# Kernel optimization log

Hardware: AMD Instinct MI355X
Metric: run time of the kernel (lower is better)

Reference implementation:

```python
import jax, jax.numpy as jnp
import numpy as np

B, T, D = 8, 2048, 1024  # batch, block_size (== seq len), n_embd


def setup_inputs() -> dict:
    key = jax.random.key(0)
    k1, k2 = jax.random.split(key)
    x = jax.random.normal(k1, (B, T, D), dtype=jnp.float32)
    W_qkv = jax.random.normal(k2, (3 * D, D), dtype=jnp.float32) * 0.02
    b_qkv = jnp.zeros((3 * D,), dtype=jnp.float32)
    ln_w = jnp.ones((D,), dtype=jnp.float32)
    ln_b = jnp.zeros((D,), dtype=jnp.float32)
    return {"x": x, "W_qkv": W_qkv, "b_qkv": b_qkv, "ln_w": ln_w, "ln_b": ln_b}


def reference(x, W_qkv, b_qkv, ln_w, ln_b):
    # qkv projection: Linear(n_embd, 3*n_embd)
    qkv = jnp.einsum('btd,ed->bte', x, W_qkv) + b_qkv  # [B,T,3D]
    q, k, v = jnp.split(qkv, 3, axis=-1)
    # causal linear attention (no softmax)
    scale = np.sqrt(D * T).astype(np.float32)
    scores = jnp.einsum('bid,bjd->bij', q, k) / scale  # [B,T,T]
    mask = jnp.tril(jnp.ones((T, T), dtype=scores.dtype))
    scores = scores * mask
    y = jnp.einsum('bij,bjd->bid', scores, v)  # [B,T,D]
    # LayerNorm over last dim, eps=1e-5
    mu = jnp.mean(y, axis=-1, keepdims=True)
    var = jnp.mean(jnp.square(y - mu), axis=-1, keepdims=True)
    y_hat = (y - mu) * jax.lax.rsqrt(var + 1e-5)
    return y_hat * ln_w + ln_b
```

## Files before the change

kernel.cpp:

```cpp
#include <hip/hip_runtime.h>
#include <hip/hip_bf16.h>
#include <stdint.h>

typedef __attribute__((ext_vector_type(8))) short bf16x8;
typedef __attribute__((ext_vector_type(4))) float f32x4;
typedef __attribute__((ext_vector_type(4))) unsigned short us4;

#define TILE_M 128
#define TILE_N 128
#define TILE_K 32

__device__ __forceinline__ unsigned short f2b(float f) {
  union { float f; unsigned u; } u;
  u.f = f;
  unsigned r = u.u + 0x7fffu + ((u.u >> 16) & 1u);
  return (unsigned short)(r >> 16);
}

__device__ __forceinline__ void gload_lds16(const void* g, void* lds) {
  __builtin_amdgcn_global_load_lds(
      (const __attribute__((address_space(1))) unsigned int*)(uintptr_t)g,
      (__attribute__((address_space(3))) unsigned int*)(uintptr_t)lds,
      16, 0, 0);
}

__device__ __forceinline__ void stage_tile(const unsigned short* __restrict__ g,
                                           long ld, long row0,
                                           unsigned short* lds, int tid) {
  int w = tid >> 6, lane = tid & 63;
#pragma unroll
  for (int j = 0; j < 2; ++j) {
    int o = ((w * 2 + j) << 10) + lane * 16;
    int row = o >> 6;
    int col = (o & 63) >> 1;
    const unsigned short* gp = g + (row0 + row) * ld + col;
    gload_lds16(gp, (char*)lds + ((w * 2 + j) << 10));
  }
}

__global__ __launch_bounds__(256, 2) void gemm1_qkv(
    const unsigned short* __restrict__ A,
    const unsigned short* __restrict__ Bm,
    const float* __restrict__ bias,
    unsigned short* __restrict__ C) {
  __shared__ unsigned short lsA[TILE_M * TILE_K];
  __shared__ unsigned short lsB[TILE_N * TILE_K];
  int tid = threadIdx.x;
  int lane = tid & 63, w = tid >> 6;
  int wr = w >> 1, wc = w & 1;
  long bm0 = (long)blockIdx.y * TILE_M;
  long bn0 = (long)blockIdx.x * TILE_N;
  f32x4 acc[4][4] = {};
  int r = lane & 15, g = lane >> 4;
  for (int kt = 0; kt < 1024 / TILE_K; ++kt) {
    long k0 = (long)kt * TILE_K;
    stage_tile(A + k0, 1024, bm0, lsA, tid);
    stage_tile(Bm + k0, 1024, bn0, lsB, tid);
    __syncthreads();
    bf16x8 aF[4], bF[4];
#pragma unroll
    for (int m = 0; m < 4; ++m)
      aF[m] = *(const bf16x8*)(lsA + (wr * 64 + m * 16 + r) * 32 + g * 8);
#pragma unroll
    for (int n = 0; n < 4; ++n)
      bF[n] = *(const bf16x8*)(lsB + (wc * 64 + n * 16 + r) * 32 + g * 8);
#pragma unroll
    for (int m = 0; m < 4; ++m)
#pragma unroll
      for (int n = 0; n < 4; ++n)
        acc[m][n] = __builtin_amdgcn_mfma_f32_16x16x32_bf16(aF[m], bF[n], acc[m][n], 0, 0, 0);
    __syncthreads();
  }
#pragma unroll
  for (int n = 0; n < 4; ++n) {
    long col = bn0 + wc * 64 + n * 16 + r;
    float bv = bias[col];
#pragma unroll
    for (int m = 0; m < 4; ++m)
#pragma unroll
      for (int j = 0; j < 4; ++j) {
        long row = bm0 + wr * 64 + m * 16 + g * 4 + j;
        C[row * 3072 + col] = f2b(acc[m][n][j] + bv);
      }
  }
}

__global__ __launch_bounds__(256, 2) void gemm2_scores(
    const unsigned short* __restrict__ qkv,
    unsigned short* __restrict__ scores,
    float inv_scale) {
  int bj = blockIdx.x, bi = blockIdx.y, b = blockIdx.z;
  if (bj > bi) return;
  __shared__ unsigned short lsA[TILE_M * TILE_K];
  __shared__ unsigned short lsB[TILE_N * TILE_K];
  int tid = threadIdx.x;
  int lane = tid & 63, w = tid >> 6;
  int wr = w >> 1, wc = w & 1;
  long bm0 = (long)bi * TILE_M;
  long bn0 = (long)bj * TILE_N;
  const unsigned short* A = qkv + (long)b * 2048 * 3072;
  const unsigned short* Bm = qkv + (long)b * 2048 * 3072 + 1024;
  f32x4 acc[4][4] = {};
  int r = lane & 15, g = lane >> 4;
  for (int kt = 0; kt < 1024 / TILE_K; ++kt) {
    long k0 = (long)kt * TILE_K;
    stage_tile(A + k0, 3072, bm0, lsA, tid);
    stage_tile(Bm + k0, 3072, bn0, lsB, tid);
    __syncthreads();
    bf16x8 aF[4], bF[4];
#pragma unroll
    for (int m = 0; m < 4; ++m)
      aF[m] = *(const bf16x8*)(lsA + (wr * 64 + m * 16 + r) * 32 + g * 8);
#pragma unroll
    for (int n = 0; n < 4; ++n)
      bF[n] = *(const bf16x8*)(lsB + (wc * 64 + n * 16 + r) * 32 + g * 8);
#pragma unroll
    for (int m = 0; m < 4; ++m)
#pragma unroll
      for (int n = 0; n < 4; ++n)
        acc[m][n] = __builtin_amdgcn_mfma_f32_16x16x32_bf16(aF[m], bF[n], acc[m][n], 0, 0, 0);
    __syncthreads();
  }
  unsigned short* S = scores + (long)b * 2048 * 2048;
#pragma unroll
  for (int n = 0; n < 4; ++n) {
    long col = bn0 + wc * 64 + n * 16 + r;
#pragma unroll
    for (int m = 0; m < 4; ++m)
#pragma unroll
      for (int j = 0; j < 4; ++j) {
        long row = bm0 + wr * 64 + m * 16 + g * 4 + j;
        float v = acc[m][n][j] * inv_scale;
        if (col > row) v = 0.0f;
        S[row * 2048 + col] = f2b(v);
      }
  }
}

__global__ __launch_bounds__(256, 2) void gemm3_y(
    const unsigned short* __restrict__ scores,
    const unsigned short* __restrict__ vT,
    float* __restrict__ out) {
  int bn = blockIdx.x, bi = blockIdx.y, b = blockIdx.z;
  __shared__ unsigned short lsA[TILE_M * TILE_K];
  __shared__ unsigned short lsB[TILE_N * TILE_K];
  int tid = threadIdx.x;
  int lane = tid & 63, w = tid >> 6;
  int wr = w >> 1, wc = w & 1;
  long bm0 = (long)bi * TILE_M;
  long bn0 = (long)bn * TILE_N;
  const unsigned short* A = scores + (long)b * 2048 * 2048;
  const unsigned short* Bm = vT + (long)b * 1024 * 2048;
  f32x4 acc[4][4] = {};
  int r = lane & 15, g = lane >> 4;
  int KT = (bi + 1) * (TILE_M / TILE_K);
  for (int kt = 0; kt < KT; ++kt) {
    long k0 = (long)kt * TILE_K;
    stage_tile(A + k0, 2048, bm0, lsA, tid);
    stage_tile(Bm + k0, 2048, bn0, lsB, tid);
    __syncthreads();
    bf16x8 aF[4], bF[4];
#pragma unroll
    for (int m = 0; m < 4; ++m)
      aF[m] = *(const bf16x8*)(lsA + (wr * 64 + m * 16 + r) * 32 + g * 8);
#pragma unroll
    for (int n = 0; n < 4; ++n)
      bF[n] = *(const bf16x8*)(lsB + (wc * 64 + n * 16 + r) * 32 + g * 8);
#pragma unroll
    for (int m = 0; m < 4; ++m)
#pragma unroll
      for (int n = 0; n < 4; ++n)
        acc[m][n] = __builtin_amdgcn_mfma_f32_16x16x32_bf16(aF[m], bF[n], acc[m][n], 0, 0, 0);
    __syncthreads();
  }
#pragma unroll
  for (int n = 0; n < 4; ++n) {
    long col = bn0 + wc * 64 + n * 16 + r;
#pragma unroll
    for (int m = 0; m < 4; ++m)
#pragma unroll
      for (int j = 0; j < 4; ++j) {
        long row = bm0 + wr * 64 + m * 16 + g * 4 + j;
        out[((long)b * 2048 + row) * 1024 + col] = acc[m][n][j];
      }
  }
}

__global__ void cvt_f32_bf16(const float* __restrict__ in,
                             unsigned short* __restrict__ out, long n) {
  long i = ((long)blockIdx.x * blockDim.x + threadIdx.x) * 8;
  if (i + 8 > n) return;
  float4 a = *(const float4*)(in + i);
  float4 b = *(const float4*)(in + i + 4);
  bf16x8 o;
  o[0] = (short)f2b(a.x); o[1] = (short)f2b(a.y);
  o[2] = (short)f2b(a.z); o[3] = (short)f2b(a.w);
  o[4] = (short)f2b(b.x); o[5] = (short)f2b(b.y);
  o[6] = (short)f2b(b.z); o[7] = (short)f2b(b.w);
  *(bf16x8*)(out + i) = o;
}

__global__ void transpose_v(const unsigned short* __restrict__ qkv,
                            unsigned short* __restrict__ vT) {
  __shared__ unsigned short tile[64][72];
  int t0 = blockIdx.x * 64, d0 = blockIdx.y * 64, b = blockIdx.z;
  int tid = threadIdx.x;
  int sub = tid & 15, grp = tid >> 4;
#pragma unroll
  for (int it = 0; it < 4; ++it) {
    int tt = it * 16 + grp;
    int dd = sub * 4;
    const unsigned short* src =
        qkv + ((long)(b * 2048 + t0 + tt)) * 3072 + 2048 + d0 + dd;
    *(us4*)&tile[tt][dd] = *(const us4*)src;
  }
  __syncthreads();
#pragma unroll
  for (int it = 0; it < 4; ++it) {
    int dd = it * 16 + grp;
    int ts = sub * 4;
    us4 o;
    o[0] = tile[ts + 0][dd];
    o[1] = tile[ts + 1][dd];
    o[2] = tile[ts + 2][dd];
    o[3] = tile[ts + 3][dd];
    *(us4*)(vT + ((long)b * 1024 + d0 + dd) * 2048 + t0 + ts) = o;
  }
}

__global__ void ln_kernel(float* __restrict__ y, const float* __restrict__ wv,
                          const float* __restrict__ bv) {
  __shared__ float sm[4];
  long row = blockIdx.x;
  int tid = threadIdx.x;
  float4 v = *(const float4*)(y + row * 1024 + tid * 4);
  float s = v.x + v.y + v.z + v.w;
#pragma unroll
  for (int o = 32; o > 0; o >>= 1) s += __shfl_xor(s, o, 64);
  if ((tid & 63) == 0) sm[tid >> 6] = s;
  __syncthreads();
  float mu = (sm[0] + sm[1] + sm[2] + sm[3]) * (1.0f / 1024.0f);
  float dx = v.x - mu, dy = v.y - mu, dz = v.z - mu, dw = v.w - mu;
  float sq = dx * dx + dy * dy + dz * dz + dw * dw;
#pragma unroll
  for (int o = 32; o > 0; o >>= 1) sq += __shfl_xor(sq, o, 64);
  __syncthreads();
  if ((tid & 63) == 0) sm[tid >> 6] = sq;
  __syncthreads();
  float var = (sm[0] + sm[1] + sm[2] + sm[3]) * (1.0f / 1024.0f);
  float inv = rsqrtf(var + 1e-5f);
  float4 w4 = *(const float4*)(wv + tid * 4);
  float4 b4 = *(const float4*)(bv + tid * 4);
  float4 o4;
  o4.x = dx * inv * w4.x + b4.x;
  o4.y = dy * inv * w4.y + b4.y;
  o4.z = dz * inv * w4.z + b4.z;
  o4.w = dw * inv * w4.w + b4.w;
  *(float4*)(y + row * 1024 + tid * 4) = o4;
}

extern "C" void kernel_launch(void* const* d_in, const int* in_sizes, int n_in,
                              void* d_out, int out_size, void* d_ws, size_t ws_size,
                              hipStream_t stream) {
  const float* x   = (const float*)d_in[0];
  const float* W   = (const float*)d_in[1];
  const float* bq  = (const float*)d_in[2];
  const float* lnw = (const float*)d_in[3];
  const float* lnb = (const float*)d_in[4];
  float* out = (float*)d_out;

  char* ws = (char*)d_ws;
  unsigned short* qkv = (unsigned short*)(ws);
  unsigned short* vT  = (unsigned short*)(ws + 100663296L);
  unsigned short* sc  = (unsigned short*)(ws + 134217728L);
  unsigned short* xb  = (unsigned short*)(ws + 134217728L);
  unsigned short* Wb  = (unsigned short*)(ws + 167772160L);

  const float inv_scale = 1.0f / sqrtf(1024.0f * 2048.0f);

  cvt_f32_bf16<<<8192, 256, 0, stream>>>(x, xb, 16384L * 1024);
  cvt_f32_bf16<<<1536, 256, 0, stream>>>(W, Wb, 3072L * 1024);
  gemm1_qkv<<<dim3(24, 128), 256, 0, stream>>>(xb, Wb, bq, qkv);
  transpose_v<<<dim3(32, 16, 8), 256, 0, stream>>>(qkv, vT);
  gemm2_scores<<<dim3(16, 16, 8), 256, 0, stream>>>(qkv, sc, inv_scale);
  gemm3_y<<<dim3(8, 16, 8), 256, 0, stream>>>(sc, vT, out);
  ln_kernel<<<16384, 256, 0, stream>>>(out, lnw, lnb);
}
```

Before: 444.2 us.

## Rewrite GEMMs with 256x256 tiles, swizzled double-buffered LDS and interleaved MFMA pipeline

All three GEMMs now share one core that uses 256x256 output tiles with 512 threads, K=64 stages, XOR-swizzled LDS to avoid bank conflicts, and a double-buffered 128 KB LDS ring. Global-to-LDS loads are issued in quarters between MFMA groups, with explicit waitcnt, barriers and raised scheduling priority so memory overlaps compute. gemm1 also remaps block ids for better L2 locality. The larger tiles cut grid sizes and raise register pressure. The causal gemm3 now has coarser load imbalance, since K is rounded up to 256-row steps.

```diff
diff --git a/kernel.cpp b/kernel.cpp
--- a/kernel.cpp
+++ b/kernel.cpp
@@ -6,9 +6,7 @@
 typedef __attribute__((ext_vector_type(4))) float f32x4;
 typedef __attribute__((ext_vector_type(4))) unsigned short us4;
 
-#define TILE_M 128
-#define TILE_N 128
-#define TILE_K 32
+#define SWZ(L) ((L) ^ ((((L) >> 7) & 7) << 4))
 
 __device__ __forceinline__ unsigned short f2b(float f) {
   union { float f; unsigned u; } u;
@@ -24,112 +22,175 @@
       16, 0, 0);
 }
 
-__device__ __forceinline__ void stage_tile(const unsigned short* __restrict__ g,
-                                           long ld, long row0,
-                                           unsigned short* lds, int tid) {
+__device__ __forceinline__ void stage_half(
+    const unsigned short* __restrict__ Ag, const unsigned short* __restrict__ Bg,
+    long bm0, long bn0, long ldA, long ldB, char* lds, int h, int tid) {
+  int T = h >> 2, q = h & 3;
+  const unsigned short* mat = (q < 2) ? Ag : Bg;
+  long row0 = (q < 2) ? bm0 : bn0;
+  long ld = (q < 2) ? ldA : ldB;
+  char* tile = lds + (long)(T & 1) * 65536 + (q >> 1) * 32768;
   int w = tid >> 6, lane = tid & 63;
 #pragma unroll
   for (int j = 0; j < 2; ++j) {
-    int o = ((w * 2 + j) << 10) + lane * 16;
-    int row = o >> 6;
-    int col = (o & 63) >> 1;
-    const unsigned short* gp = g + (row0 + row) * ld + col;
-    gload_lds16(gp, (char*)lds + ((w * 2 + j) << 10));
-  }
-}
-
-__global__ __launch_bounds__(256, 2) void gemm1_qkv(
-    const unsigned short* __restrict__ A,
-    const unsigned short* __restrict__ Bm,
-    const float* __restrict__ bias,
-    unsigned short* __restrict__ C) {
-  __shared__ unsigned short lsA[TILE_M * TILE_K];
-  __shared__ unsigned short lsB[TILE_N * TILE_K];
+    int P = (q & 1) * 16384 + j * 8192 + w * 1024 + lane * 16;
+    int L = SWZ(P);
+    const unsigned short* gp =
+        mat + (row0 + (L >> 7)) * ld + (long)T * 64 + ((L & 127) >> 1);
+    gload_lds16(gp, tile + (q & 1) * 16384 + j * 8192 + w * 1024);
+  }
+}
+
+__device__ __forceinline__ void readA(const char* tA, int wr, int r, int g,
+                                      bf16x8 (&aF)[8][2]) {
+#pragma unroll
+  for (int m = 0; m < 8; ++m)
+#pragma unroll
+    for (int s = 0; s < 2; ++s) {
+      int L = (wr * 128 + m * 16 + r) * 128 + s * 64 + g * 16;
+      aF[m][s] = *(const bf16x8*)(tA + SWZ(L));
+    }
+}
+
+__device__ __forceinline__ void readB(const char* tB, int wc, int qn, int r, int g,
+                                      bf16x8 (&bF)[2][2]) {
+#pragma unroll
+  for (int n = 0; n < 2; ++n)
+#pragma unroll
+    for (int s = 0; s < 2; ++s) {
+      int L = (wc * 64 + (qn * 2 + n) * 16 + r) * 128 + s * 64 + g * 16;
+      bF[n][s] = *(const bf16x8*)(tB + SWZ(L));
+    }
+}
+
+template <int QM, int QN>
+__device__ __forceinline__ void mfma_quad(f32x4 (&acc)[8][4], bf16x8 (&aF)[8][2],
+                                          bf16x8 (&bF)[2][2]) {
+#pragma unroll
+  for (int s = 0; s < 2; ++s)
+#pragma unroll
+    for (int mm = 0; mm < 4; ++mm)
+#pragma unroll
+      for (int nn = 0; nn < 2; ++nn)
+        acc[QM * 4 + mm][QN * 2 + nn] = __builtin_amdgcn_mfma_f32_16x16x32_bf16(
+            aF[QM * 4 + mm][s], bF[nn][s], acc[QM * 4 + mm][QN * 2 + nn], 0, 0, 0);
+}
+
+#define SBAR() do { __builtin_amdgcn_s_barrier(); __builtin_amdgcn_sched_barrier(0); } while (0)
+
+__device__ __forceinline__ void gemm_core(
+    const unsigned short* __restrict__ Ag, const unsigned short* __restrict__ Bg,
+    long bm0, long bn0, long ldA, long ldB, int KT, char* lds,
+    f32x4 (&acc)[8][4]) {
   int tid = threadIdx.x;
-  int lane = tid & 63, w = tid >> 6;
-  int wr = w >> 1, wc = w & 1;
-  long bm0 = (long)blockIdx.y * TILE_M;
-  long bn0 = (long)blockIdx.x * TILE_N;
-  f32x4 acc[4][4] = {};
+  int w = tid >> 6, lane = tid & 63;
+  int wr = w >> 2, wc = w & 3;
   int r = lane & 15, g = lane >> 4;
-  for (int kt = 0; kt < 1024 / TILE_K; ++kt) {
-    long k0 = (long)kt * TILE_K;
-    stage_tile(A + k0, 1024, bm0, lsA, tid);
-    stage_tile(Bm + k0, 1024, bn0, lsB, tid);
-    __syncthreads();
-    bf16x8 aF[4], bF[4];
-#pragma unroll
-    for (int m = 0; m < 4; ++m)
-      aF[m] = *(const bf16x8*)(lsA + (wr * 64 + m * 16 + r) * 32 + g * 8);
-#pragma unroll
-    for (int n = 0; n < 4; ++n)
-      bF[n] = *(const bf16x8*)(lsB + (wc * 64 + n * 16 + r) * 32 + g * 8);
-#pragma unroll
-    for (int m = 0; m < 4; ++m)
-#pragma unroll
-      for (int n = 0; n < 4; ++n)
-        acc[m][n] = __builtin_amdgcn_mfma_f32_16x16x32_bf16(aF[m], bF[n], acc[m][n], 0, 0, 0);
-    __syncthreads();
-  }
+  int totalH = KT * 4;
+#pragma unroll
+  for (int h = 0; h < 7; ++h)
+    stage_half(Ag, Bg, bm0, bn0, ldA, ldB, lds, h, tid);
+  asm volatile("s_waitcnt vmcnt(6)" ::: "memory");
+  SBAR();
+
+  bf16x8 aF[8][2], bF[2][2];
+  int niter = KT >> 1;
+  for (int it = 0; it < niter; ++it) {
+    bool last = (it == niter - 1);
+    int hb = it * 8 + 7;
+#pragma unroll
+    for (int c = 0; c < 2; ++c) {
+      char* tA = lds + c * 65536;
+      char* tB = tA + 32768;
+      readA(tA, wr, r, g, aF);
+      readB(tB, wc, 0, r, g, bF);
+      if (hb + c * 4 + 0 < totalH)
+        stage_half(Ag, Bg, bm0, bn0, ldA, ldB, lds, hb + c * 4 + 0, tid);
+      SBAR();
+      __builtin_amdgcn_s_setprio(1);
+      mfma_quad<0, 0>(acc, aF, bF);
+      __builtin_amdgcn_s_setprio(0);
+      asm volatile("s_waitcnt lgkmcnt(0)" ::: "memory");
+      __builtin_amdgcn_sched_barrier(0);
+      SBAR();
+      if (hb + c * 4 + 1 < totalH)
+        stage_half(Ag, Bg, bm0, bn0, ldA, ldB, lds, hb + c * 4 + 1, tid);
+      SBAR();
+      __builtin_amdgcn_s_setprio(1);
+      mfma_quad<1, 0>(acc, aF, bF);
+      __builtin_amdgcn_s_setprio(0);
+      SBAR();
+      readB(tB, wc, 1, r, g, bF);
+      if (hb + c * 4 + 2 < totalH)
+        stage_half(Ag, Bg, bm0, bn0, ldA, ldB, lds, hb + c * 4 + 2, tid);
+      SBAR();
+      __builtin_amdgcn_s_setprio(1);
+      mfma_quad<1, 1>(acc, aF, bF);
+      __builtin_amdgcn_s_setprio(0);
+      SBAR();
+      if (hb + c * 4 + 3 < totalH)
+        stage_half(Ag, Bg, bm0, bn0, ldA, ldB, lds, hb + c * 4 + 3, tid);
+      SBAR();
+      __builtin_amdgcn_s_setprio(1);
+      mfma_quad<0, 1>(acc, aF, bF);
+      __builtin_amdgcn_s_setprio(0);
+      if (!last)
+        asm volatile("s_waitcnt vmcnt(6)" ::: "memory");
+      else if (c == 0)
+        asm volatile("s_waitcnt vmcnt(0)" ::: "memory");
+      SBAR();
+    }
+  }
+}
+
+__global__ __launch_bounds__(512, 2) void gemm1_qkv(
+    const unsigned short* __restrict__ A, const unsigned short* __restrict__ Bm,
+    const float* __restrict__ bias, unsigned short* __restrict__ C) {
+  extern __shared__ char smem[];
+  int bid = blockIdx.x;
+  int s = (bid & 7) * 96 + (bid >> 3);
+  long bm0 = (long)(s / 12) * 256;
+  long bn0 = (long)(s % 12) * 256;
+  f32x4 acc[8][4] = {};
+  gemm_core(A, Bm, bm0, bn0, 1024, 1024, 16, smem, acc);
+  int tid = threadIdx.x, w = tid >> 6, lane = tid & 63;
+  int wr = w >> 2, wc = w & 3, r = lane & 15, g = lane >> 4;
 #pragma unroll
   for (int n = 0; n < 4; ++n) {
     long col = bn0 + wc * 64 + n * 16 + r;
     float bv = bias[col];
 #pragma unroll
-    for (int m = 0; m < 4; ++m)
+    for (int m = 0; m < 8; ++m)
 #pragma unroll
       for (int j = 0; j < 4; ++j) {
-        long row = bm0 + wr * 64 + m * 16 + g * 4 + j;
+        long row = bm0 + wr * 128 + m * 16 + g * 4 + j;
         C[row * 3072 + col] = f2b(acc[m][n][j] + bv);
       }
   }
 }
 
-__global__ __launch_bounds__(256, 2) void gemm2_scores(
-    const unsigned short* __restrict__ qkv,
-    unsigned short* __restrict__ scores,
+__global__ __launch_bounds__(512, 2) void gemm2_scores(
+    const unsigned short* __restrict__ qkv, unsigned short* __restrict__ scores,
     float inv_scale) {
+  extern __shared__ char smem[];
   int bj = blockIdx.x, bi = blockIdx.y, b = blockIdx.z;
   if (bj > bi) return;
-  __shared__ unsigned short lsA[TILE_M * TILE_K];
-  __shared__ unsigned short lsB[TILE_N * TILE_K];
-  int tid = threadIdx.x;
-  int lane = tid & 63, w = tid >> 6;
-  int wr = w >> 1, wc = w & 1;
-  long bm0 = (long)bi * TILE_M;
-  long bn0 = (long)bj * TILE_N;
   const unsigned short* A = qkv + (long)b * 2048 * 3072;
-  const unsigned short* Bm = qkv + (long)b * 2048 * 3072 + 1024;
-  f32x4 acc[4][4] = {};
-  int r = lane & 15, g = lane >> 4;
-  for (int kt = 0; kt < 1024 / TILE_K; ++kt) {
-    long k0 = (long)kt * TILE_K;
-    stage_tile(A + k0, 3072, bm0, lsA, tid);
-    stage_tile(Bm + k0, 3072, bn0, lsB, tid);
-    __syncthreads();
-    bf16x8 aF[4], bF[4];
-#pragma unroll
-    for (int m = 0; m < 4; ++m)
-      aF[m] = *(const bf16x8*)(lsA + (wr * 64 + m * 16 + r) * 32 + g * 8);
-#pragma unroll
-    for (int n = 0; n < 4; ++n)
-      bF[n] = *(const bf16x8*)(lsB + (wc * 64 + n * 16 + r) * 32 + g * 8);
-#pragma unroll
-    for (int m = 0; m < 4; ++m)
-#pragma unroll
-      for (int n = 0; n < 4; ++n)
-        acc[m][n] = __builtin_amdgcn_mfma_f32_16x16x32_bf16(aF[m], bF[n], acc[m][n], 0, 0, 0);
-    __syncthreads();
-  }
+  const unsigned short* Bm = A + 1024;
+  long bm0 = (long)bi * 256, bn0 = (long)bj * 256;
+  f32x4 acc[8][4] = {};
+  gemm_core(A, Bm, bm0, bn0, 3072, 3072, 16, smem, acc);
   unsigned short* S = scores + (long)b * 2048 * 2048;
+  int tid = threadIdx.x, w = tid >> 6, lane = tid & 63;
+  int wr = w >> 2, wc = w & 3, r = lane & 15, g = lane >> 4;
 #pragma unroll
   for (int n = 0; n < 4; ++n) {
     long col = bn0 + wc * 64 + n * 16 + r;
 #pragma unroll
-    for (int m = 0; m < 4; ++m)
+    for (int m = 0; m < 8; ++m)
 #pragma unroll
       for (int j = 0; j < 4; ++j) {
-        long row = bm0 + wr * 64 + m * 16 + g * 4 + j;
+        long row = bm0 + wr * 128 + m * 16 + g * 4 + j;
         float v = acc[m][n][j] * inv_scale;
         if (col > row) v = 0.0f;
         S[row * 2048 + col] = f2b(v);
@@ -137,50 +198,26 @@
   }
 }
 
-__global__ __launch_bounds__(256, 2) void gemm3_y(
-    const unsigned short* __restrict__ scores,
-    const unsigned short* __restrict__ vT,
+__global__ __launch_bounds__(512, 2) void gemm3_y(
+    const unsigned short* __restrict__ scores, const unsigned short* __restrict__ vT,
     float* __restrict__ out) {
+  extern __shared__ char smem[];
   int bn = blockIdx.x, bi = blockIdx.y, b = blockIdx.z;
-  __shared__ unsigned short lsA[TILE_M * TILE_K];
-  __shared__ unsigned short lsB[TILE_N * TILE_K];
-  int tid = threadIdx.x;
-  int lane = tid & 63, w = tid >> 6;
-  int wr = w >> 1, wc = w & 1;
-  long bm0 = (long)bi * TILE_M;
-  long bn0 = (long)bn * TILE_N;
   const unsigned short* A = scores + (long)b * 2048 * 2048;
   const unsigned short* Bm = vT + (long)b * 1024 * 2048;
-  f32x4 acc[4][4] = {};
-  int r = lane & 15, g = lane >> 4;
-  int KT = (bi + 1) * (TILE_M / TILE_K);
-  for (int kt = 0; kt < KT; ++kt) {
-    long k0 = (long)kt * TILE_K;
-    stage_tile(A + k0, 2048, bm0, lsA, tid);
-    stage_tile(Bm + k0, 2048, bn0, lsB, tid);
-    __syncthreads();
-    bf16x8 aF[4], bF[4];
-#pragma unroll
-    for (int m = 0; m < 4; ++m)
-      aF[m] = *(const bf16x8*)(lsA + (wr * 64 + m * 16 + r) * 32 + g * 8);
-#pragma unroll
-    for (int n = 0; n < 4; ++n)
-      bF[n] = *(const bf16x8*)(lsB + (wc * 64 + n * 16 + r) * 32 + g * 8);
-#pragma unroll
-    for (int m = 0; m < 4; ++m)
-#pragma unroll
-      for (int n = 0; n < 4; ++n)
-        acc[m][n] = __builtin_amdgcn_mfma_f32_16x16x32_bf16(aF[m], bF[n], acc[m][n], 0, 0, 0);
-    __syncthreads();
-  }
+  long bm0 = (long)bi * 256, bn0 = (long)bn * 256;
+  f32x4 acc[8][4] = {};
+  gemm_core(A, Bm, bm0, bn0, 2048, 2048, (bi + 1) * 4, smem, acc);
+  int tid = threadIdx.x, w = tid >> 6, lane = tid & 63;
+  int wr = w >> 2, wc = w & 3, r = lane & 15, g = lane >> 4;
 #pragma unroll
   for (int n = 0; n < 4; ++n) {
     long col = bn0 + wc * 64 + n * 16 + r;
 #pragma unroll
-    for (int m = 0; m < 4; ++m)
+    for (int m = 0; m < 8; ++m)
 #pragma unroll
       for (int j = 0; j < 4; ++j) {
-        long row = bm0 + wr * 64 + m * 16 + g * 4 + j;
+        long row = bm0 + wr * 128 + m * 16 + g * 4 + j;
         out[((long)b * 2048 + row) * 1024 + col] = acc[m][n][j];
       }
   }
@@ -262,27 +299,34 @@
 extern "C" void kernel_launch(void* const* d_in, const int* in_sizes, int n_in,
                               void* d_out, int out_size, void* d_ws, size_t ws_size,
                               hipStream_t stream) {
-  const float* x   = (const float*)d_in[0];
-  const float* W   = (const float*)d_in[1];
-  const float* bq  = (const float*)d_in[2];
+  const float* x = (const float*)d_in[0];
+  const float* W = (const float*)d_in[1];
+  const float* bq = (const float*)d_in[2];
   const float* lnw = (const float*)d_in[3];
   const float* lnb = (const float*)d_in[4];
   float* out = (float*)d_out;
 
   char* ws = (char*)d_ws;
   unsigned short* qkv = (unsigned short*)(ws);
-  unsigned short* vT  = (unsigned short*)(ws + 100663296L);
-  unsigned short* sc  = (unsigned short*)(ws + 134217728L);
-  unsigned short* xb  = (unsigned short*)(ws + 134217728L);
-  unsigned short* Wb  = (unsigned short*)(ws + 167772160L);
+  unsigned short* vT = (unsigned short*)(ws + 100663296L);
+  unsigned short* sc = (unsigned short*)(ws + 134217728L);
+  unsigned short* xb = (unsigned short*)(ws + 134217728L);
+  unsigned short* Wb = (unsigned short*)(ws + 167772160L);
 
   const float inv_scale = 1.0f / sqrtf(1024.0f * 2048.0f);
+
+  hipFuncSetAttribute((const void*)gemm1_qkv,
+                      hipFuncAttributeMaxDynamicSharedMemorySize, 131072);
+  hipFuncSetAttribute((const void*)gemm2_scores,
+                      hipFuncAttributeMaxDynamicSharedMemorySize, 131072);
+  hipFuncSetAttribute((const void*)gemm3_y,
+                      hipFuncAttributeMaxDynamicSharedMemorySize, 131072);
 
   cvt_f32_bf16<<<8192, 256, 0, stream>>>(x, xb, 16384L * 1024);
   cvt_f32_bf16<<<1536, 256, 0, stream>>>(W, Wb, 3072L * 1024);
-  gemm1_qkv<<<dim3(24, 128), 256, 0, stream>>>(xb, Wb, bq, qkv);
+  gemm1_qkv<<<768, 512, 131072, stream>>>(xb, Wb, bq, qkv);
   transpose_v<<<dim3(32, 16, 8), 256, 0, stream>>>(qkv, vT);
-  gemm2_scores<<<dim3(16, 16, 8), 256, 0, stream>>>(qkv, sc, inv_scale);
-  gemm3_y<<<dim3(8, 16, 8), 256, 0, stream>>>(sc, vT, out);
+  gemm2_scores<<<dim3(8, 8, 8), 512, 131072, stream>>>(qkv, sc, inv_scale);
+  gemm3_y<<<dim3(4, 8, 8), 512, 131072, stream>>>(sc, vT, out);
   ln_kernel<<<16384, 256, 0, stream>>>(out, lnw, lnb);
 }
```

After: 865.4 us. +94.8%, slower.

## Split QKV into separate buffers, compact causal grid, heavy-first block ordering

Applied to the files above, without the earlier changes.

The QKV projection now writes Q, K and V into three contiguous [B*T,1024] buffers instead of one interleaved [B*T,3072] buffer, so later kernels read with a 1024 stride. The scores kernel launches only the 136 lower-triangular tiles per batch, mapping a linear index back to (bi,bj) with a small loop, instead of launching 256 and exiting early on the upper half. Both the scores and output GEMMs now schedule the largest-row (most work) tiles first to reduce tail imbalance. The index decode adds a short serial loop per block.

```diff
diff --git a/kernel.cpp b/kernel.cpp
--- a/kernel.cpp
+++ b/kernel.cpp
@@ -5,10 +5,6 @@
 typedef __attribute__((ext_vector_type(8))) short bf16x8;
 typedef __attribute__((ext_vector_type(4))) float f32x4;
 typedef __attribute__((ext_vector_type(4))) unsigned short us4;
-
-#define TILE_M 128
-#define TILE_N 128
-#define TILE_K 32
 
 __device__ __forceinline__ unsigned short f2b(float f) {
   union { float f; unsigned u; } u;
@@ -23,6 +19,9 @@
       (__attribute__((address_space(3))) unsigned int*)(uintptr_t)lds,
       16, 0, 0);
 }
+
+#define TILE_M 128
+#define TILE_K 32
 
 __device__ __forceinline__ void stage_tile(const unsigned short* __restrict__ g,
                                            long ld, long row0,
@@ -42,14 +41,15 @@
     const unsigned short* __restrict__ A,
     const unsigned short* __restrict__ Bm,
     const float* __restrict__ bias,
-    unsigned short* __restrict__ C) {
+    unsigned short* __restrict__ qb, unsigned short* __restrict__ kb,
+    unsigned short* __restrict__ vb) {
   __shared__ unsigned short lsA[TILE_M * TILE_K];
-  __shared__ unsigned short lsB[TILE_N * TILE_K];
+  __shared__ unsigned short lsB[TILE_M * TILE_K];
   int tid = threadIdx.x;
   int lane = tid & 63, w = tid >> 6;
   int wr = w >> 1, wc = w & 1;
   long bm0 = (long)blockIdx.y * TILE_M;
-  long bn0 = (long)blockIdx.x * TILE_N;
+  long bn0 = (long)blockIdx.x * TILE_M;
   f32x4 acc[4][4] = {};
   int r = lane & 15, g = lane >> 4;
   for (int kt = 0; kt < 1024 / TILE_K; ++kt) {
@@ -71,41 +71,46 @@
         acc[m][n] = __builtin_amdgcn_mfma_f32_16x16x32_bf16(aF[m], bF[n], acc[m][n], 0, 0, 0);
     __syncthreads();
   }
+  int part = blockIdx.x >> 3;
+  unsigned short* O = (part == 0) ? qb : (part == 1) ? kb : vb;
+  long cl0 = (long)(blockIdx.x & 7) * 128;
 #pragma unroll
   for (int n = 0; n < 4; ++n) {
-    long col = bn0 + wc * 64 + n * 16 + r;
-    float bv = bias[col];
+    long cc = wc * 64 + n * 16 + r;
+    float bv = bias[bn0 + cc];
 #pragma unroll
     for (int m = 0; m < 4; ++m)
 #pragma unroll
       for (int j = 0; j < 4; ++j) {
         long row = bm0 + wr * 64 + m * 16 + g * 4 + j;
-        C[row * 3072 + col] = f2b(acc[m][n][j] + bv);
+        O[row * 1024 + cl0 + cc] = f2b(acc[m][n][j] + bv);
       }
   }
 }
 
 __global__ __launch_bounds__(256, 2) void gemm2_scores(
-    const unsigned short* __restrict__ qkv,
-    unsigned short* __restrict__ scores,
-    float inv_scale) {
-  int bj = blockIdx.x, bi = blockIdx.y, b = blockIdx.z;
-  if (bj > bi) return;
+    const unsigned short* __restrict__ qm, const unsigned short* __restrict__ km,
+    unsigned short* __restrict__ scores, float inv_scale) {
   __shared__ unsigned short lsA[TILE_M * TILE_K];
-  __shared__ unsigned short lsB[TILE_N * TILE_K];
+  __shared__ unsigned short lsB[TILE_M * TILE_K];
+  int p = 135 - blockIdx.x;
+  int bi = 0, base = 0;
+  while (p >= base + bi + 1) { base += bi + 1; ++bi; }
+  int bj = p - base;
+  int b = blockIdx.y;
   int tid = threadIdx.x;
   int lane = tid & 63, w = tid >> 6;
   int wr = w >> 1, wc = w & 1;
   long bm0 = (long)bi * TILE_M;
-  long bn0 = (long)bj * TILE_N;
-  const unsigned short* A = qkv + (long)b * 2048 * 3072;
-  const unsigned short* Bm = qkv + (long)b * 2048 * 3072 + 1024;
+  long bn0 = (long)bj * TILE_M;
+  const unsigned short* A = qm + (long)b * 2048 * 1024;
+  const unsigned short* Bm = km + (long)b * 2048 * 1024;
   f32x4 acc[4][4] = {};
   int r = lane & 15, g = lane >> 4;
   for (int kt = 0; kt < 1024 / TILE_K; ++kt) {
     long k0 = (long)kt * TILE_K;
-    stage_tile(A + k0, 3072, bm0, lsA, tid);
-    stage_tile(Bm + k0, 3072, bn0, lsB, tid);
+    stage_tile(A + k0, 1024, bm0, lsA, tid);
+    stage_tile(Bm + k0, 1024, bn0, lsB, tid);
     __syncthreads();
     bf16x8 aF[4], bF[4];
 #pragma unroll
@@ -138,17 +143,16 @@
 }
 
 __global__ __launch_bounds__(256, 2) void gemm3_y(
-    const unsigned short* __restrict__ scores,
-    const unsigned short* __restrict__ vT,
+    const unsigned short* __restrict__ scores, const unsigned short* __restrict__ vT,
     float* __restrict__ out) {
-  int bn = blockIdx.x, bi = blockIdx.y, b = blockIdx.z;
   __shared__ unsigned short lsA[TILE_M * TILE_K];
-  __shared__ unsigned short lsB[TILE_N * TILE_K];
+  __shared__ unsigned short lsB[TILE_M * TILE_K];
+  int bn = blockIdx.x, bi = 15 - blockIdx.y, b = blockIdx.z;
   int tid = threadIdx.x;
   int lane = tid & 63, w = tid >> 6;
   int wr = w >> 1, wc = w & 1;
   long bm0 = (long)bi * TILE_M;
-  long bn0 = (long)bn * TILE_N;
+  long bn0 = (long)bn * TILE_M;
   const unsigned short* A = scores + (long)b * 2048 * 2048;
   const unsigned short* Bm = vT + (long)b * 1024 * 2048;
   f32x4 acc[4][4] = {};
@@ -200,7 +204,7 @@
   *(bf16x8*)(out + i) = o;
 }
 
-__global__ void transpose_v(const unsigned short* __restrict__ qkv,
+__global__ void transpose_v(const unsigned short* __restrict__ vm,
                             unsigned short* __restrict__ vT) {
   __shared__ unsigned short tile[64][72];
   int t0 = blockIdx.x * 64, d0 = blockIdx.y * 64, b = blockIdx.z;
@@ -211,7 +215,7 @@
     int tt = it * 16 + grp;
     int dd = sub * 4;
     const unsigned short* src =
-        qkv + ((long)(b * 2048 + t0 + tt)) * 3072 + 2048 + d0 + dd;
+        vm + ((long)(b * 2048 + t0 + tt)) * 1024 + d0 + dd;
     *(us4*)&tile[tt][dd] = *(const us4*)src;
   }
   __syncthreads();
@@ -262,27 +266,29 @@
 extern "C" void kernel_launch(void* const* d_in, const int* in_sizes, int n_in,
                               void* d_out, int out_size, void* d_ws, size_t ws_size,
                               hipStream_t stream) {
-  const float* x   = (const float*)d_in[0];
-  const float* W   = (const float*)d_in[1];
-  const float* bq  = (const float*)d_in[2];
+  const float* x = (const float*)d_in[0];
+  const float* W = (const float*)d_in[1];
+  const float* bq = (const float*)d_in[2];
   const float* lnw = (const float*)d_in[3];
   const float* lnb = (const float*)d_in[4];
   float* out = (float*)d_out;
 
   char* ws = (char*)d_ws;
-  unsigned short* qkv = (unsigned short*)(ws);
-  unsigned short* vT  = (unsigned short*)(ws + 100663296L);
-  unsigned short* sc  = (unsigned short*)(ws + 134217728L);
-  unsigned short* xb  = (unsigned short*)(ws + 134217728L);
-  unsigned short* Wb  = (unsigned short*)(ws + 167772160L);
+  unsigned short* qb = (unsigned short*)(ws);
+  unsigned short* kb = (unsigned short*)(ws + 33554432L);
+  unsigned short* vb = (unsigned short*)(ws + 67108864L);
+  unsigned short* vT = (unsigned short*)(ws + 100663296L);
+  unsigned short* xb = (unsigned short*)(ws + 134217728L);
+  unsigned short* Wb = (unsigned short*)(ws + 167772160L);
+  unsigned short* sc = (unsigned short*)(ws + 134217728L);
 
   const float inv_scale = 1.0f / sqrtf(1024.0f * 2048.0f);
 
   cvt_f32_bf16<<<8192, 256, 0, stream>>>(x, xb, 16384L * 1024);
   cvt_f32_bf16<<<1536, 256, 0, stream>>>(W, Wb, 3072L * 1024);
-  gemm1_qkv<<<dim3(24, 128), 256, 0, stream>>>(xb, Wb, bq, qkv);
-  transpose_v<<<dim3(32, 16, 8), 256, 0, stream>>>(qkv, vT);
-  gemm2_scores<<<dim3(16, 16, 8), 256, 0, stream>>>(qkv, sc, inv_scale);
+  gemm1_qkv<<<dim3(24, 128), 256, 0, stream>>>(xb, Wb, bq, qb, kb, vb);
+  transpose_v<<<dim3(32, 16, 8), 256, 0, stream>>>(vb, vT);
+  gemm2_scores<<<dim3(136, 8), 256, 0, stream>>>(qb, kb, sc, inv_scale);
   gemm3_y<<<dim3(8, 16, 8), 256, 0, stream>>>(sc, vT, out);
   ln_kernel<<<16384, 256, 0, stream>>>(out, lnw, lnb);
 }
```

After: 448.6 us. Within noise of the previous version (+1.0%).
